# Optimization experiments

Measured on AMD Instinct MI355X. Metric: run time of the kernel, lower is better.

## Reference

```python
import jax, jax.numpy as jnp
import numpy as np

B, S, D = 4, 2048, 512
H, DK, DV = 8, 64, 64
ALPHA = 0.6
MAX_ITERS = 3
EPS = 1e-9


def setup_inputs() -> dict:
    key = jax.random.key(0)
    ks = jax.random.split(key, 9)
    scale = 1.0 / np.sqrt(D)
    return {
        "x": jax.random.normal(ks[0], (B, S, D), dtype=jnp.float32),
        "Wq": jax.random.normal(ks[1], (D, H * DK), dtype=jnp.float32) * scale,
        "bq": jnp.zeros((H * DK,), dtype=jnp.float32),
        "Wk": jax.random.normal(ks[2], (D, H * DK), dtype=jnp.float32) * scale,
        "bk": jnp.zeros((H * DK,), dtype=jnp.float32),
        "Wv": jax.random.normal(ks[3], (D, H * DV), dtype=jnp.float32) * scale,
        "bv": jnp.zeros((H * DV,), dtype=jnp.float32),
        "Wo": jax.random.normal(ks[4], (H * DV, D), dtype=jnp.float32) * scale,
        "bo": jnp.zeros((D,), dtype=jnp.float32),
    }


def reference(x, Wq, bq, Wk, bk, Wv, bv, Wo, bo):
    # QKV projections -> [B, H, S, dk]
    q = (x @ Wq + bq).reshape(B, S, H, DK).transpose(0, 2, 1, 3)
    k = (x @ Wk + bk).reshape(B, S, H, DK).transpose(0, 2, 1, 3)
    v = (x @ Wv + bv).reshape(B, S, H, DV).transpose(0, 2, 1, 3)

    # scaled dot-product scores: [B, H, S, S]
    scores = jnp.einsum("bhqd,bhkd->bhqk", q, k) / jnp.sqrt(jnp.float32(DK))
    w = jax.nn.softmax(scores, axis=-1)

    # iterative sparsification: threshold_t = 1 / (alpha^t * N), then renormalize
    n = jnp.float32(S)
    for t in range(MAX_ITERS):
        thr = 1.0 / ((ALPHA ** t) * n)
        w = jnp.where(w >= thr, w, 0.0)
        w = w / (jnp.sum(w, axis=-1, keepdims=True) + EPS)

    # attend and project out
    out = jnp.einsum("bhqk,bhkd->bhqd", w, v)          # [B, H, S, dv]
    out = out.transpose(0, 2, 1, 3).reshape(B, S, H * DV)
    return out @ Wo + bo
```

## Files before the change

kernel.cpp:

```cpp
#include <hip/hip_runtime.h>
#include <hip/hip_bf16.h>
#include <math.h>

#define NB 4
#define NS 2048
#define ND 512
#define NH 8
#define NDK 64
#define NDV 64

typedef __attribute__((ext_vector_type(8))) short short8;
typedef __attribute__((ext_vector_type(4))) float f32x4;

__device__ __forceinline__ unsigned short f2bfu(float f) {
  unsigned int u = __builtin_bit_cast(unsigned int, f);
  unsigned int rounding = 0x7fffu + ((u >> 16) & 1u);
  return (unsigned short)((u + rounding) >> 16);
}
__device__ __forceinline__ float bfu2f(unsigned short u) {
  return __builtin_bit_cast(float, (unsigned int)u << 16);
}


__global__ void k_make_xcat(const float* __restrict__ in, unsigned short* __restrict__ out,
                            int n4) {
  int i = blockIdx.x * 256 + threadIdx.x;
  if (i >= n4) return;
  int row = i >> 7, col = (i & 127) * 4;
  float4 f = reinterpret_cast<const float4*>(in)[i];
  ushort4 h, l;
  h.x = f2bfu(f.x); h.y = f2bfu(f.y); h.z = f2bfu(f.z); h.w = f2bfu(f.w);
  l.x = f2bfu(f.x - bfu2f(h.x)); l.y = f2bfu(f.y - bfu2f(h.y));
  l.z = f2bfu(f.z - bfu2f(h.z)); l.w = f2bfu(f.w - bfu2f(h.w));
  ushort4* o = reinterpret_cast<ushort4*>(out + (size_t)row * 1536);
  o[col / 4] = h;
  o[(col + 512) / 4] = h;
  o[(col + 1024) / 4] = l;
}

__global__ void k_transpose_split(const float* __restrict__ src, unsigned short* __restrict__ dst,
                                  int R, int C) {
  __shared__ float t[32][33];
  int bx = blockIdx.x * 32, by = blockIdx.y * 32;
  int tx = threadIdx.x, ty = threadIdx.y;
  for (int i = 0; i < 32; i += 8)
    t[ty + i][tx] = src[(size_t)(by + ty + i) * C + bx + tx];
  __syncthreads();
  for (int i = 0; i < 32; i += 8) {
    float f = t[tx][ty + i];
    unsigned short h = f2bfu(f);
    unsigned short l = f2bfu(f - bfu2f(h));
    size_t base = (size_t)(bx + ty + i) * (3 * R) + by + tx;
    dst[base] = h;
    dst[base + R] = l;
    dst[base + 2 * R] = h;
  }
}

template <int MODE>
__global__ __launch_bounds__(256) void k_gemm_nt(
    const unsigned short* __restrict__ A, const unsigned short* __restrict__ Bt,
    const float* __restrict__ bias, void* __restrict__ outp, unsigned short* __restrict__ outlo,
    int M, int N, int K) {
  __shared__ __align__(16) unsigned short As[64][88];
  __shared__ __align__(16) unsigned short Bs[64][88];
  const int tid = threadIdx.x;
  const int m0 = blockIdx.y * 64;
  const int n0 = blockIdx.x * 64;
  const int wave = tid >> 6, lane = tid & 63;
  const int lm = lane & 15, lg = lane >> 4;

  f32x4 acc[4];
  for (int n = 0; n < 4; n++) acc[n] = (f32x4){0.f, 0.f, 0.f, 0.f};

  for (int k0 = 0; k0 < K; k0 += 64) {
    for (int it = 0; it < 2; it++) {
      int c = tid + it * 256;
      int row = c >> 3, col = (c & 7) * 8;
      *reinterpret_cast<short8*>(&As[row][col]) =
          *reinterpret_cast<const short8*>(A + (size_t)(m0 + row) * K + k0 + col);
      *reinterpret_cast<short8*>(&Bs[row][col]) =
          *reinterpret_cast<const short8*>(Bt + (size_t)(n0 + row) * K + k0 + col);
    }
    __syncthreads();
#pragma unroll
    for (int ks = 0; ks < 2; ks++) {
      short8 a = *reinterpret_cast<const short8*>(&As[wave * 16 + lm][ks * 32 + lg * 8]);
#pragma unroll
      for (int n = 0; n < 4; n++) {
        short8 b = *reinterpret_cast<const short8*>(&Bs[n * 16 + lm][ks * 32 + lg * 8]);
        acc[n] = __builtin_amdgcn_mfma_f32_16x16x32_bf16(a, b, acc[n], 0, 0, 0);
      }
    }
    __syncthreads();
  }

#pragma unroll
  for (int n = 0; n < 4; n++) {
    int gn = n0 + n * 16 + lm;
    float bv = bias[gn];
#pragma unroll
    for (int r = 0; r < 4; r++) {
      int gm = m0 + wave * 16 + lg * 4 + r;
      float v = acc[n][r] + bv;
      if (MODE == 3) {
        reinterpret_cast<float*>(outp)[(size_t)gm * ND + gn] = v;
      } else {
        int b = gm >> 11, s = gm & (NS - 1);
        int h = gn >> 6, d = gn & 63;
        unsigned short hb = f2bfu(v);
        unsigned short lb = f2bfu(v - bfu2f(hb));
        size_t idx;
        if (MODE == 0)
          idx = (((size_t)b * NH + h) * NS + s) * NDK + d;
        else
          idx = (((size_t)b * NH + h) * NDV + d) * NS + s;
        reinterpret_cast<unsigned short*>(outp)[idx] = hb;
        outlo[idx] = lb;
      }
    }
  }
}

__global__ __launch_bounds__(1024) void k_sparse_attn(
    const unsigned short* __restrict__ Qh, const unsigned short* __restrict__ Ql,
    const unsigned short* __restrict__ Kh, const unsigned short* __restrict__ Kl,
    const unsigned short* __restrict__ Vth, const unsigned short* __restrict__ Vtl,
    unsigned short* __restrict__ attn) {
  __shared__ __align__(16) float sc[16][2052];
  __shared__ __align__(16) float red[4][4][16][16];
  __shared__ float rowcut[16], rowinv[16];

  const int tid = threadIdx.x;
  const int wave = tid >> 6, lane = tid & 63;
  const int lm = lane & 15, lg = lane >> 4;

  const int orig = blockIdx.x;
  const int blk = (orig & 7) * 512 + (orig >> 3);
  const int qt = blk & (NS / 16 - 1);
  const int bh = blk >> 7;
  const int q0 = qt * 16;

  const size_t qoff = ((size_t)bh * NS + q0) * NDK;
  const unsigned short* Kph = Kh + (size_t)bh * NS * NDK;
  const unsigned short* Kpl = Kl + (size_t)bh * NS * NDK;
  const unsigned short* Vph = Vth + (size_t)bh * NDV * NS;
  const unsigned short* Vpl = Vtl + (size_t)bh * NDV * NS;

  {
    short8 qh0 = *reinterpret_cast<const short8*>(Qh + qoff + lm * NDK + lg * 8);
    short8 qh1 = *reinterpret_cast<const short8*>(Qh + qoff + lm * NDK + 32 + lg * 8);
    short8 ql0 = *reinterpret_cast<const short8*>(Ql + qoff + lm * NDK + lg * 8);
    short8 ql1 = *reinterpret_cast<const short8*>(Ql + qoff + lm * NDK + 32 + lg * 8);
#pragma unroll
    for (int it = 0; it < 8; it++) {
      int t0 = wave * 128 + it * 16;
      f32x4 a = (f32x4){0.f, 0.f, 0.f, 0.f};
      size_t ko = (size_t)t0 * NDK;
      short8 bh0 = *reinterpret_cast<const short8*>(Kph + ko + lm * NDK + lg * 8);
      short8 bh1 = *reinterpret_cast<const short8*>(Kph + ko + lm * NDK + 32 + lg * 8);
      short8 bl0 = *reinterpret_cast<const short8*>(Kpl + ko + lm * NDK + lg * 8);
      short8 bl1 = *reinterpret_cast<const short8*>(Kpl + ko + lm * NDK + 32 + lg * 8);
      a = __builtin_amdgcn_mfma_f32_16x16x32_bf16(qh0, bh0, a, 0, 0, 0);
      a = __builtin_amdgcn_mfma_f32_16x16x32_bf16(qh1, bh1, a, 0, 0, 0);
      a = __builtin_amdgcn_mfma_f32_16x16x32_bf16(qh0, bl0, a, 0, 0, 0);
      a = __builtin_amdgcn_mfma_f32_16x16x32_bf16(qh1, bl1, a, 0, 0, 0);
      a = __builtin_amdgcn_mfma_f32_16x16x32_bf16(ql0, bh0, a, 0, 0, 0);
      a = __builtin_amdgcn_mfma_f32_16x16x32_bf16(ql1, bh1, a, 0, 0, 0);
#pragma unroll
      for (int r = 0; r < 4; r++)
        sc[lg * 4 + r][t0 + lm] = a[r] * 0.125f;
    }
  }
  __syncthreads();

  {
    const float thr[3] = {1.0f / 2048.0f, 1.0f / (0.6f * 2048.0f), 1.0f / (0.36f * 2048.0f)};
    const int row = wave;
    float m = -1e30f;
    for (int i = lane; i < NS; i += 64) m = fmaxf(m, sc[row][i]);
    for (int s = 32; s > 0; s >>= 1) m = fmaxf(m, __shfl_xor(m, s));
    float E = 0.f;
    for (int i = lane; i < NS; i += 64) {
      float e = __expf(sc[row][i] - m);
      sc[row][i] = e;
      E += e;
    }
    for (int s = 32; s > 0; s >>= 1) E += __shfl_xor(E, s);
    float Dd = 1.0f, cutE = 0.f;
#pragma unroll
    for (int t = 0; t < 3; t++) {
      cutE = fmaxf(cutE, thr[t] * Dd * E);
      float Ssum = 0.f;
      for (int i = lane; i < NS; i += 64) {
        float e = sc[row][i];
        if (e >= cutE) Ssum += e;
      }
      for (int s = 32; s > 0; s >>= 1) Ssum += __shfl_xor(Ssum, s);
      Dd = Ssum / E + 1e-9f * Dd;
    }
    if (lane == 0) {
      rowcut[row] = cutE;
      rowinv[row] = 1.0f / (E * Dd);
    }
  }
  __syncthreads();

  {
    const int d = wave & 3;
    const int kk = wave >> 2;
    const float cut = rowcut[lm], inv = rowinv[lm];
    const unsigned short* vph = Vph + (size_t)(d * 16 + lm) * NS + kk * 512;
    const unsigned short* vpl = Vpl + (size_t)(d * 16 + lm) * NS + kk * 512;
    f32x4 pacc = (f32x4){0.f, 0.f, 0.f, 0.f};
#pragma unroll
    for (int ks = 0; ks < 16; ks++) {
      int c = kk * 512 + ks * 32 + lg * 8;
      f32x4 e0 = *reinterpret_cast<const f32x4*>(&sc[lm][c]);
      f32x4 e1 = *reinterpret_cast<const f32x4*>(&sc[lm][c + 4]);
      short8 ah, al;
#pragma unroll
      for (int j = 0; j < 4; j++) {
        float w0 = (e0[j] >= cut) ? e0[j] * inv : 0.f;
        unsigned short h0 = f2bfu(w0);
        ah[j] = (short)h0; al[j] = (short)f2bfu(w0 - bfu2f(h0));
        float w1 = (e1[j] >= cut) ? e1[j] * inv : 0.f;
        unsigned short h1 = f2bfu(w1);
        ah[4 + j] = (short)h1; al[4 + j] = (short)f2bfu(w1 - bfu2f(h1));
      }
      short8 vh = *reinterpret_cast<const short8*>(vph + ks * 32 + lg * 8);
      short8 vl = *reinterpret_cast<const short8*>(vpl + ks * 32 + lg * 8);
      pacc = __builtin_amdgcn_mfma_f32_16x16x32_bf16(ah, vh, pacc, 0, 0, 0);
      pacc = __builtin_amdgcn_mfma_f32_16x16x32_bf16(ah, vl, pacc, 0, 0, 0);
      pacc = __builtin_amdgcn_mfma_f32_16x16x32_bf16(al, vh, pacc, 0, 0, 0);
    }
#pragma unroll
    for (int r = 0; r < 4; r++) red[kk][d][lg * 4 + r][lm] = pacc[r];
  }
  __syncthreads();

  if (wave < 4) {
    const int d = wave;
    const int b = bh >> 3, h = bh & 7;
#pragma unroll
    for (int r = 0; r < 4; r++) {
      int q = lg * 4 + r;
      float v = red[0][d][q][lm] + red[1][d][q][lm] + red[2][d][q][lm] + red[3][d][q][lm];
      int s = q0 + q;
      int c = h * 64 + d * 16 + lm;
      unsigned short hb = f2bfu(v);
      unsigned short lb = f2bfu(v - bfu2f(hb));
      size_t base = ((size_t)b * NS + s) * 1536;
      attn[base + c] = hb;
      attn[base + c + 512] = hb;
      attn[base + c + 1024] = lb;
    }
  }
}


extern "C" void kernel_launch(void* const* d_in, const int* in_sizes, int n_in,
                              void* d_out, int out_size, void* d_ws, size_t ws_size,
                              hipStream_t stream) {
  const float* x  = (const float*)d_in[0];
  const float* Wq = (const float*)d_in[1];
  const float* bq = (const float*)d_in[2];
  const float* Wk = (const float*)d_in[3];
  const float* bk = (const float*)d_in[4];
  const float* Wv = (const float*)d_in[5];
  const float* bv = (const float*)d_in[6];
  const float* Wo = (const float*)d_in[7];
  const float* bo = (const float*)d_in[8];

  char* ws = (char*)d_ws;
  size_t off = 0;
  auto alloc = [&](size_t bytes) {
    char* p = ws + off;
    off += (bytes + 255) & ~(size_t)255;
    return p;
  };
  const int M = NB * NS;
  unsigned short* xcat = (unsigned short*)alloc((size_t)M * 1536 * 2);
  unsigned short* wqC  = (unsigned short*)alloc((size_t)512 * 1536 * 2);
  unsigned short* wkC  = (unsigned short*)alloc((size_t)512 * 1536 * 2);
  unsigned short* wvC  = (unsigned short*)alloc((size_t)512 * 1536 * 2);
  unsigned short* woC  = (unsigned short*)alloc((size_t)512 * 1536 * 2);
  unsigned short* Qhi  = (unsigned short*)alloc((size_t)M * 512 * 2);
  unsigned short* Qlo  = (unsigned short*)alloc((size_t)M * 512 * 2);
  unsigned short* Khi  = (unsigned short*)alloc((size_t)M * 512 * 2);
  unsigned short* Klo  = (unsigned short*)alloc((size_t)M * 512 * 2);
  unsigned short* Vthi = (unsigned short*)alloc((size_t)M * 512 * 2);
  unsigned short* Vtlo = (unsigned short*)alloc((size_t)M * 512 * 2);
  unsigned short* attn = xcat;

  k_make_xcat<<<(M * 512 / 4 + 255) / 256, 256, 0, stream>>>(x, xcat, M * 512 / 4);

  dim3 tg(16, 16), tb(32, 8);
  k_transpose_split<<<tg, tb, 0, stream>>>(Wq, wqC, ND, NH * NDK);
  k_transpose_split<<<tg, tb, 0, stream>>>(Wk, wkC, ND, NH * NDK);
  k_transpose_split<<<tg, tb, 0, stream>>>(Wv, wvC, ND, NH * NDV);
  k_transpose_split<<<tg, tb, 0, stream>>>(Wo, woC, NH * NDV, ND);

  dim3 gg(512 / 64, M / 64);
  k_gemm_nt<0><<<gg, 256, 0, stream>>>(xcat, wqC, bq, Qhi, Qlo, M, 512, 1536);
  k_gemm_nt<0><<<gg, 256, 0, stream>>>(xcat, wkC, bk, Khi, Klo, M, 512, 1536);
  k_gemm_nt<2><<<gg, 256, 0, stream>>>(xcat, wvC, bv, Vthi, Vtlo, M, 512, 1536);

  k_sparse_attn<<<NB * NH * (NS / 16), 1024, 0, stream>>>(Qhi, Qlo, Khi, Klo, Vthi, Vtlo, attn);

  k_gemm_nt<3><<<gg, 256, 0, stream>>>(attn, woC, bo, d_out, nullptr, M, 512, 1536);
}
```

Baseline: 976.1 us.

## Keep softmax rows in registers and precompute split-bf16 probabilities in LDS

Each wave now loads its score row into registers once and does the max, exp, and three threshold passes without rereading shared memory. The normalized, split-bf16 probabilities are written back into the score buffer, so the PV stage reads them directly instead of recomputing the threshold and conversion in every wave. The QK stage swaps the MFMA operands to get vectorized f32x4 stores, and both matmul stages use independent accumulators to break MFMA dependency chains. The cost is higher register pressure from holding 32 floats per lane at 1024 threads per block.

```diff
diff --git a/kernel.cpp b/kernel.cpp
--- a/kernel.cpp
+++ b/kernel.cpp
@@ -129,7 +129,6 @@
     unsigned short* __restrict__ attn) {
   __shared__ __align__(16) float sc[16][2052];
   __shared__ __align__(16) float red[4][4][16][16];
-  __shared__ float rowcut[16], rowinv[16];
 
   const int tid = threadIdx.x;
   const int wave = tid >> 6, lane = tid & 63;
@@ -153,55 +152,97 @@
     short8 ql0 = *reinterpret_cast<const short8*>(Ql + qoff + lm * NDK + lg * 8);
     short8 ql1 = *reinterpret_cast<const short8*>(Ql + qoff + lm * NDK + 32 + lg * 8);
 #pragma unroll
-    for (int it = 0; it < 8; it++) {
-      int t0 = wave * 128 + it * 16;
-      f32x4 a = (f32x4){0.f, 0.f, 0.f, 0.f};
-      size_t ko = (size_t)t0 * NDK;
-      short8 bh0 = *reinterpret_cast<const short8*>(Kph + ko + lm * NDK + lg * 8);
-      short8 bh1 = *reinterpret_cast<const short8*>(Kph + ko + lm * NDK + 32 + lg * 8);
-      short8 bl0 = *reinterpret_cast<const short8*>(Kpl + ko + lm * NDK + lg * 8);
-      short8 bl1 = *reinterpret_cast<const short8*>(Kpl + ko + lm * NDK + 32 + lg * 8);
-      a = __builtin_amdgcn_mfma_f32_16x16x32_bf16(qh0, bh0, a, 0, 0, 0);
-      a = __builtin_amdgcn_mfma_f32_16x16x32_bf16(qh1, bh1, a, 0, 0, 0);
-      a = __builtin_amdgcn_mfma_f32_16x16x32_bf16(qh0, bl0, a, 0, 0, 0);
-      a = __builtin_amdgcn_mfma_f32_16x16x32_bf16(qh1, bl1, a, 0, 0, 0);
-      a = __builtin_amdgcn_mfma_f32_16x16x32_bf16(ql0, bh0, a, 0, 0, 0);
-      a = __builtin_amdgcn_mfma_f32_16x16x32_bf16(ql1, bh1, a, 0, 0, 0);
-#pragma unroll
-      for (int r = 0; r < 4; r++)
-        sc[lg * 4 + r][t0 + lm] = a[r] * 0.125f;
+    for (int it = 0; it < 8; it += 2) {
+      int t0a = wave * 128 + it * 16;
+      int t0b = t0a + 16;
+      size_t koa = (size_t)t0a * NDK, kob = (size_t)t0b * NDK;
+      short8 ah0 = *reinterpret_cast<const short8*>(Kph + koa + lm * NDK + lg * 8);
+      short8 ah1 = *reinterpret_cast<const short8*>(Kph + koa + lm * NDK + 32 + lg * 8);
+      short8 al0 = *reinterpret_cast<const short8*>(Kpl + koa + lm * NDK + lg * 8);
+      short8 al1 = *reinterpret_cast<const short8*>(Kpl + koa + lm * NDK + 32 + lg * 8);
+      short8 bh0 = *reinterpret_cast<const short8*>(Kph + kob + lm * NDK + lg * 8);
+      short8 bh1 = *reinterpret_cast<const short8*>(Kph + kob + lm * NDK + 32 + lg * 8);
+      short8 bl0 = *reinterpret_cast<const short8*>(Kpl + kob + lm * NDK + lg * 8);
+      short8 bl1 = *reinterpret_cast<const short8*>(Kpl + kob + lm * NDK + 32 + lg * 8);
+      {
+        f32x4 a0 = (f32x4){0.f, 0.f, 0.f, 0.f};
+        f32x4 a1 = (f32x4){0.f, 0.f, 0.f, 0.f};
+        a0 = __builtin_amdgcn_mfma_f32_16x16x32_bf16(ah0, qh0, a0, 0, 0, 0);
+        a1 = __builtin_amdgcn_mfma_f32_16x16x32_bf16(ah1, qh1, a1, 0, 0, 0);
+        a0 = __builtin_amdgcn_mfma_f32_16x16x32_bf16(al0, qh0, a0, 0, 0, 0);
+        a1 = __builtin_amdgcn_mfma_f32_16x16x32_bf16(al1, qh1, a1, 0, 0, 0);
+        a0 = __builtin_amdgcn_mfma_f32_16x16x32_bf16(ah0, ql0, a0, 0, 0, 0);
+        a1 = __builtin_amdgcn_mfma_f32_16x16x32_bf16(ah1, ql1, a1, 0, 0, 0);
+        f32x4 v = (a0 + a1) * 0.125f;
+        *reinterpret_cast<f32x4*>(&sc[lm][t0a + lg * 4]) = v;
+      }
+      {
+        f32x4 a0 = (f32x4){0.f, 0.f, 0.f, 0.f};
+        f32x4 a1 = (f32x4){0.f, 0.f, 0.f, 0.f};
+        a0 = __builtin_amdgcn_mfma_f32_16x16x32_bf16(bh0, qh0, a0, 0, 0, 0);
+        a1 = __builtin_amdgcn_mfma_f32_16x16x32_bf16(bh1, qh1, a1, 0, 0, 0);
+        a0 = __builtin_amdgcn_mfma_f32_16x16x32_bf16(bl0, qh0, a0, 0, 0, 0);
+        a1 = __builtin_amdgcn_mfma_f32_16x16x32_bf16(bl1, qh1, a1, 0, 0, 0);
+        a0 = __builtin_amdgcn_mfma_f32_16x16x32_bf16(bh0, ql0, a0, 0, 0, 0);
+        a1 = __builtin_amdgcn_mfma_f32_16x16x32_bf16(bh1, ql1, a1, 0, 0, 0);
+        f32x4 v = (a0 + a1) * 0.125f;
+        *reinterpret_cast<f32x4*>(&sc[lm][t0b + lg * 4]) = v;
+      }
     }
   }
   __syncthreads();
 
   {
     const float thr[3] = {1.0f / 2048.0f, 1.0f / (0.6f * 2048.0f), 1.0f / (0.36f * 2048.0f)};
-    const int row = wave;
+    char* rb = (char*)&sc[wave][0];
+    f32x4 ev[8];
+#pragma unroll
+    for (int it = 0; it < 8; it++)
+      ev[it] = *reinterpret_cast<const f32x4*>(rb + 4 * (it * 256 + lane * 4));
     float m = -1e30f;
-    for (int i = lane; i < NS; i += 64) m = fmaxf(m, sc[row][i]);
+#pragma unroll
+    for (int it = 0; it < 8; it++)
+      m = fmaxf(m, fmaxf(fmaxf(ev[it][0], ev[it][1]), fmaxf(ev[it][2], ev[it][3])));
     for (int s = 32; s > 0; s >>= 1) m = fmaxf(m, __shfl_xor(m, s));
     float E = 0.f;
-    for (int i = lane; i < NS; i += 64) {
-      float e = __expf(sc[row][i] - m);
-      sc[row][i] = e;
-      E += e;
+#pragma unroll
+    for (int it = 0; it < 8; it++) {
+#pragma unroll
+      for (int j = 0; j < 4; j++) {
+        float e = __expf(ev[it][j] - m);
+        ev[it][j] = e;
+        E += e;
+      }
     }
     for (int s = 32; s > 0; s >>= 1) E += __shfl_xor(E, s);
-    float Dd = 1.0f, cutE = 0.f;
+    float Dd = 1.0f, cut = 0.f;
 #pragma unroll
     for (int t = 0; t < 3; t++) {
-      cutE = fmaxf(cutE, thr[t] * Dd * E);
+      cut = fmaxf(cut, thr[t] * Dd * E);
       float Ssum = 0.f;
-      for (int i = lane; i < NS; i += 64) {
-        float e = sc[row][i];
-        if (e >= cutE) Ssum += e;
+#pragma unroll
+      for (int it = 0; it < 8; it++) {
+#pragma unroll
+        for (int j = 0; j < 4; j++) Ssum += (ev[it][j] >= cut) ? ev[it][j] : 0.f;
       }
       for (int s = 32; s > 0; s >>= 1) Ssum += __shfl_xor(Ssum, s);
       Dd = Ssum / E + 1e-9f * Dd;
     }
-    if (lane == 0) {
-      rowcut[row] = cutE;
-      rowinv[row] = 1.0f / (E * Dd);
+    const float inv = 1.0f / (E * Dd);
+#pragma unroll
+    for (int it = 0; it < 8; it++) {
+      ushort4 hv, lv;
+#pragma unroll
+      for (int j = 0; j < 4; j++) {
+        float e = ev[it][j];
+        float w = (e >= cut) ? e * inv : 0.f;
+        unsigned short h = f2bfu(w);
+        (&hv.x)[j] = h;
+        (&lv.x)[j] = f2bfu(w - bfu2f(h));
+      }
+      int c = it * 256 + lane * 4;
+      *reinterpret_cast<ushort4*>(rb + 2 * c) = hv;
+      *reinterpret_cast<ushort4*>(rb + 4096 + 2 * c) = lv;
     }
   }
   __syncthreads();
@@ -209,31 +250,31 @@
   {
     const int d = wave & 3;
     const int kk = wave >> 2;
-    const float cut = rowcut[lm], inv = rowinv[lm];
     const unsigned short* vph = Vph + (size_t)(d * 16 + lm) * NS + kk * 512;
     const unsigned short* vpl = Vpl + (size_t)(d * 16 + lm) * NS + kk * 512;
-    f32x4 pacc = (f32x4){0.f, 0.f, 0.f, 0.f};
-#pragma unroll
-    for (int ks = 0; ks < 16; ks++) {
-      int c = kk * 512 + ks * 32 + lg * 8;
-      f32x4 e0 = *reinterpret_cast<const f32x4*>(&sc[lm][c]);
-      f32x4 e1 = *reinterpret_cast<const f32x4*>(&sc[lm][c + 4]);
-      short8 ah, al;
-#pragma unroll
-      for (int j = 0; j < 4; j++) {
-        float w0 = (e0[j] >= cut) ? e0[j] * inv : 0.f;
-        unsigned short h0 = f2bfu(w0);
-        ah[j] = (short)h0; al[j] = (short)f2bfu(w0 - bfu2f(h0));
-        float w1 = (e1[j] >= cut) ? e1[j] * inv : 0.f;
-        unsigned short h1 = f2bfu(w1);
-        ah[4 + j] = (short)h1; al[4 + j] = (short)f2bfu(w1 - bfu2f(h1));
-      }
-      short8 vh = *reinterpret_cast<const short8*>(vph + ks * 32 + lg * 8);
-      short8 vl = *reinterpret_cast<const short8*>(vpl + ks * 32 + lg * 8);
-      pacc = __builtin_amdgcn_mfma_f32_16x16x32_bf16(ah, vh, pacc, 0, 0, 0);
-      pacc = __builtin_amdgcn_mfma_f32_16x16x32_bf16(ah, vl, pacc, 0, 0, 0);
-      pacc = __builtin_amdgcn_mfma_f32_16x16x32_bf16(al, vh, pacc, 0, 0, 0);
-    }
+    const char* prow = (const char*)&sc[lm][0];
+    f32x4 acc0 = (f32x4){0.f, 0.f, 0.f, 0.f};
+    f32x4 acc1 = (f32x4){0.f, 0.f, 0.f, 0.f};
+    f32x4 acc2 = (f32x4){0.f, 0.f, 0.f, 0.f};
+#pragma unroll
+    for (int ks = 0; ks < 16; ks += 2) {
+      int c0 = kk * 512 + ks * 32 + lg * 8;
+      short8 vh0 = *reinterpret_cast<const short8*>(vph + ks * 32 + lg * 8);
+      short8 vl0 = *reinterpret_cast<const short8*>(vpl + ks * 32 + lg * 8);
+      short8 vh1 = *reinterpret_cast<const short8*>(vph + (ks + 1) * 32 + lg * 8);
+      short8 vl1 = *reinterpret_cast<const short8*>(vpl + (ks + 1) * 32 + lg * 8);
+      short8 ph0 = *reinterpret_cast<const short8*>(prow + 2 * c0);
+      short8 pl0 = *reinterpret_cast<const short8*>(prow + 4096 + 2 * c0);
+      short8 ph1 = *reinterpret_cast<const short8*>(prow + 2 * (c0 + 32));
+      short8 pl1 = *reinterpret_cast<const short8*>(prow + 4096 + 2 * (c0 + 32));
+      acc0 = __builtin_amdgcn_mfma_f32_16x16x32_bf16(ph0, vh0, acc0, 0, 0, 0);
+      acc1 = __builtin_amdgcn_mfma_f32_16x16x32_bf16(ph0, vl0, acc1, 0, 0, 0);
+      acc2 = __builtin_amdgcn_mfma_f32_16x16x32_bf16(pl0, vh0, acc2, 0, 0, 0);
+      acc0 = __builtin_amdgcn_mfma_f32_16x16x32_bf16(ph1, vh1, acc0, 0, 0, 0);
+      acc1 = __builtin_amdgcn_mfma_f32_16x16x32_bf16(ph1, vl1, acc1, 0, 0, 0);
+      acc2 = __builtin_amdgcn_mfma_f32_16x16x32_bf16(pl1, vh1, acc2, 0, 0, 0);
+    }
+    f32x4 pacc = (acc0 + acc1) + acc2;
 #pragma unroll
     for (int r = 0; r < 4; r++) red[kk][d][lg * 4 + r][lm] = pacc[r];
   }
```

Result: faster. 899.6 us (-7.8%).

## Keep attention scores in registers and drop the 128KB shared score buffer

Applied to the files above, without the earlier changes.

The sparse attention kernel no longer stages the 16x2048 score tile in shared memory. Each of 8 waves keeps its 256-key slice of transposed scores in registers, and cross-wave max, sum and threshold reductions go through a small shared partial buffer. The P matrix is rearranged into MFMA operand layout with lane shuffles, and each wave computes all 64 output dims over its key slice before a shared reduction. Freeing shared memory lets several blocks share a CU, in exchange for higher register pressure, more barriers and many shuffles.

```diff
diff --git a/kernel.cpp b/kernel.cpp
--- a/kernel.cpp
+++ b/kernel.cpp
@@ -11,6 +11,7 @@
 
 typedef __attribute__((ext_vector_type(8))) short short8;
 typedef __attribute__((ext_vector_type(4))) float f32x4;
+typedef __attribute__((ext_vector_type(4))) unsigned int u32x4;
 
 __device__ __forceinline__ unsigned short f2bfu(float f) {
   unsigned int u = __builtin_bit_cast(unsigned int, f);
@@ -122,14 +123,13 @@
   }
 }
 
-__global__ __launch_bounds__(1024) void k_sparse_attn(
+__global__ __launch_bounds__(512, 4) void k_sparse_attn(
     const unsigned short* __restrict__ Qh, const unsigned short* __restrict__ Ql,
     const unsigned short* __restrict__ Kh, const unsigned short* __restrict__ Kl,
     const unsigned short* __restrict__ Vth, const unsigned short* __restrict__ Vtl,
     unsigned short* __restrict__ attn) {
-  __shared__ __align__(16) float sc[16][2052];
-  __shared__ __align__(16) float red[4][4][16][16];
-  __shared__ float rowcut[16], rowinv[16];
+  __shared__ float part[5][8][16];
+  __shared__ __align__(16) float red[8][16][68];
 
   const int tid = threadIdx.x;
   const int wave = tid >> 6, lane = tid & 63;
@@ -146,111 +146,168 @@
   const unsigned short* Kpl = Kl + (size_t)bh * NS * NDK;
   const unsigned short* Vph = Vth + (size_t)bh * NDV * NS;
   const unsigned short* Vpl = Vtl + (size_t)bh * NDV * NS;
-
+  const int kvbase = wave * 256;
+
+  f32x4 st[16];
   {
     short8 qh0 = *reinterpret_cast<const short8*>(Qh + qoff + lm * NDK + lg * 8);
     short8 qh1 = *reinterpret_cast<const short8*>(Qh + qoff + lm * NDK + 32 + lg * 8);
     short8 ql0 = *reinterpret_cast<const short8*>(Ql + qoff + lm * NDK + lg * 8);
     short8 ql1 = *reinterpret_cast<const short8*>(Ql + qoff + lm * NDK + 32 + lg * 8);
 #pragma unroll
-    for (int it = 0; it < 8; it++) {
-      int t0 = wave * 128 + it * 16;
-      f32x4 a = (f32x4){0.f, 0.f, 0.f, 0.f};
-      size_t ko = (size_t)t0 * NDK;
-      short8 bh0 = *reinterpret_cast<const short8*>(Kph + ko + lm * NDK + lg * 8);
-      short8 bh1 = *reinterpret_cast<const short8*>(Kph + ko + lm * NDK + 32 + lg * 8);
-      short8 bl0 = *reinterpret_cast<const short8*>(Kpl + ko + lm * NDK + lg * 8);
-      short8 bl1 = *reinterpret_cast<const short8*>(Kpl + ko + lm * NDK + 32 + lg * 8);
-      a = __builtin_amdgcn_mfma_f32_16x16x32_bf16(qh0, bh0, a, 0, 0, 0);
-      a = __builtin_amdgcn_mfma_f32_16x16x32_bf16(qh1, bh1, a, 0, 0, 0);
-      a = __builtin_amdgcn_mfma_f32_16x16x32_bf16(qh0, bl0, a, 0, 0, 0);
-      a = __builtin_amdgcn_mfma_f32_16x16x32_bf16(qh1, bl1, a, 0, 0, 0);
-      a = __builtin_amdgcn_mfma_f32_16x16x32_bf16(ql0, bh0, a, 0, 0, 0);
-      a = __builtin_amdgcn_mfma_f32_16x16x32_bf16(ql1, bh1, a, 0, 0, 0);
-#pragma unroll
-      for (int r = 0; r < 4; r++)
-        sc[lg * 4 + r][t0 + lm] = a[r] * 0.125f;
-    }
+    for (int kt = 0; kt < 16; kt++) {
+      size_t ko = (size_t)(kvbase + kt * 16) * NDK;
+      const unsigned short* kh = Kph + ko + lm * NDK + lg * 8;
+      const unsigned short* kl = Kpl + ko + lm * NDK + lg * 8;
+      short8 ah0 = *reinterpret_cast<const short8*>(kh);
+      short8 ah1 = *reinterpret_cast<const short8*>(kh + 32);
+      short8 al0 = *reinterpret_cast<const short8*>(kl);
+      short8 al1 = *reinterpret_cast<const short8*>(kl + 32);
+      f32x4 a0 = (f32x4){0.f, 0.f, 0.f, 0.f};
+      f32x4 a1 = (f32x4){0.f, 0.f, 0.f, 0.f};
+      a0 = __builtin_amdgcn_mfma_f32_16x16x32_bf16(ah0, qh0, a0, 0, 0, 0);
+      a1 = __builtin_amdgcn_mfma_f32_16x16x32_bf16(ah1, qh1, a1, 0, 0, 0);
+      a0 = __builtin_amdgcn_mfma_f32_16x16x32_bf16(al0, qh0, a0, 0, 0, 0);
+      a1 = __builtin_amdgcn_mfma_f32_16x16x32_bf16(al1, qh1, a1, 0, 0, 0);
+      a0 = __builtin_amdgcn_mfma_f32_16x16x32_bf16(ah0, ql0, a0, 0, 0, 0);
+      a1 = __builtin_amdgcn_mfma_f32_16x16x32_bf16(ah1, ql1, a1, 0, 0, 0);
+      st[kt] = (a0 + a1) * 0.125f;
+    }
+  }
+
+  float cut, inv;
+  {
+    float m = -1e30f;
+#pragma unroll
+    for (int kt = 0; kt < 16; kt++)
+      m = fmaxf(m, fmaxf(fmaxf(st[kt][0], st[kt][1]), fmaxf(st[kt][2], st[kt][3])));
+    m = fmaxf(m, __shfl_xor(m, 16));
+    m = fmaxf(m, __shfl_xor(m, 32));
+    if (lg == 0) part[0][wave][lm] = m;
+    __syncthreads();
+    float gm = -1e30f;
+#pragma unroll
+    for (int w = 0; w < 8; w++) gm = fmaxf(gm, part[0][w][lm]);
+
+    float E = 0.f;
+#pragma unroll
+    for (int kt = 0; kt < 16; kt++) {
+#pragma unroll
+      for (int j = 0; j < 4; j++) {
+        float e = __expf(st[kt][j] - gm);
+        st[kt][j] = e;
+        E += e;
+      }
+    }
+    E += __shfl_xor(E, 16);
+    E += __shfl_xor(E, 32);
+    if (lg == 0) part[1][wave][lm] = E;
+    __syncthreads();
+    float gE = 0.f;
+#pragma unroll
+    for (int w = 0; w < 8; w++) gE += part[1][w][lm];
+
+    const float thr[3] = {1.0f / 2048.0f, 1.0f / (0.6f * 2048.0f), 1.0f / (0.36f * 2048.0f)};
+    float Dd = 1.0f;
+    cut = 0.f;
+#pragma unroll
+    for (int t = 0; t < 3; t++) {
+      cut = fmaxf(cut, thr[t] * Dd * gE);
+      float S = 0.f;
+#pragma unroll
+      for (int kt = 0; kt < 16; kt++) {
+#pragma unroll
+        for (int j = 0; j < 4; j++) S += (st[kt][j] >= cut) ? st[kt][j] : 0.f;
+      }
+      S += __shfl_xor(S, 16);
+      S += __shfl_xor(S, 32);
+      if (lg == 0) part[2 + t][wave][lm] = S;
+      __syncthreads();
+      float gS = 0.f;
+#pragma unroll
+      for (int w = 0; w < 8; w++) gS += part[2 + t][w][lm];
+      Dd = gS / gE + 1e-9f * Dd;
+    }
+    inv = 1.0f / (gE * Dd);
+  }
+
+  unsigned int Hp[16][2], Lp[16][2];
+#pragma unroll
+  for (int kt = 0; kt < 16; kt++) {
+#pragma unroll
+    for (int rp = 0; rp < 2; rp++) {
+      float w0 = st[kt][2 * rp], w1 = st[kt][2 * rp + 1];
+      w0 = (w0 >= cut) ? w0 * inv : 0.f;
+      w1 = (w1 >= cut) ? w1 * inv : 0.f;
+      unsigned int h0 = f2bfu(w0), h1 = f2bfu(w1);
+      Hp[kt][rp] = h0 | (h1 << 16);
+      unsigned int l0 = f2bfu(w0 - bfu2f((unsigned short)h0));
+      unsigned int l1 = f2bfu(w1 - bfu2f((unsigned short)h1));
+      Lp[kt][rp] = l0 | (l1 << 16);
+    }
+  }
+
+  {
+    const int e_lane = lm + 32 * (lg & 1);
+    const int o_lane = e_lane + 16;
+    const bool selB = (lane & 32) != 0;
+    f32x4 acc[4];
+#pragma unroll
+    for (int dt = 0; dt < 4; dt++) acc[dt] = (f32x4){0.f, 0.f, 0.f, 0.f};
+#pragma unroll
+    for (int wi = 0; wi < 8; wi++) {
+      unsigned int a0 = (unsigned)__shfl((int)Hp[2 * wi][0], e_lane);
+      unsigned int a1 = (unsigned)__shfl((int)Hp[2 * wi][1], e_lane);
+      unsigned int a2 = (unsigned)__shfl((int)Hp[2 * wi][0], o_lane);
+      unsigned int a3 = (unsigned)__shfl((int)Hp[2 * wi][1], o_lane);
+      unsigned int b0 = (unsigned)__shfl((int)Hp[2 * wi + 1][0], e_lane);
+      unsigned int b1 = (unsigned)__shfl((int)Hp[2 * wi + 1][1], e_lane);
+      unsigned int b2 = (unsigned)__shfl((int)Hp[2 * wi + 1][0], o_lane);
+      unsigned int b3 = (unsigned)__shfl((int)Hp[2 * wi + 1][1], o_lane);
+      u32x4 hw = (u32x4){selB ? b0 : a0, selB ? b1 : a1, selB ? b2 : a2, selB ? b3 : a3};
+      a0 = (unsigned)__shfl((int)Lp[2 * wi][0], e_lane);
+      a1 = (unsigned)__shfl((int)Lp[2 * wi][1], e_lane);
+      a2 = (unsigned)__shfl((int)Lp[2 * wi][0], o_lane);
+      a3 = (unsigned)__shfl((int)Lp[2 * wi][1], o_lane);
+      b0 = (unsigned)__shfl((int)Lp[2 * wi + 1][0], e_lane);
+      b1 = (unsigned)__shfl((int)Lp[2 * wi + 1][1], e_lane);
+      b2 = (unsigned)__shfl((int)Lp[2 * wi + 1][0], o_lane);
+      b3 = (unsigned)__shfl((int)Lp[2 * wi + 1][1], o_lane);
+      u32x4 lw = (u32x4){selB ? b0 : a0, selB ? b1 : a1, selB ? b2 : a2, selB ? b3 : a3};
+      short8 Ah = __builtin_bit_cast(short8, hw);
+      short8 Al = __builtin_bit_cast(short8, lw);
+      const int co = kvbase + wi * 32 + lg * 8;
+#pragma unroll
+      for (int dt = 0; dt < 4; dt++) {
+        short8 V0 = *reinterpret_cast<const short8*>(Vph + (size_t)(dt * 16 + lm) * NS + co);
+        short8 V1 = *reinterpret_cast<const short8*>(Vpl + (size_t)(dt * 16 + lm) * NS + co);
+        acc[dt] = __builtin_amdgcn_mfma_f32_16x16x32_bf16(Ah, V0, acc[dt], 0, 0, 0);
+        acc[dt] = __builtin_amdgcn_mfma_f32_16x16x32_bf16(Ah, V1, acc[dt], 0, 0, 0);
+        acc[dt] = __builtin_amdgcn_mfma_f32_16x16x32_bf16(Al, V0, acc[dt], 0, 0, 0);
+      }
+    }
+#pragma unroll
+    for (int dt = 0; dt < 4; dt++)
+#pragma unroll
+      for (int rr = 0; rr < 4; rr++) red[wave][lg * 4 + rr][dt * 16 + lm] = acc[dt][rr];
   }
   __syncthreads();
 
   {
-    const float thr[3] = {1.0f / 2048.0f, 1.0f / (0.6f * 2048.0f), 1.0f / (0.36f * 2048.0f)};
-    const int row = wave;
-    float m = -1e30f;
-    for (int i = lane; i < NS; i += 64) m = fmaxf(m, sc[row][i]);
-    for (int s = 32; s > 0; s >>= 1) m = fmaxf(m, __shfl_xor(m, s));
-    float E = 0.f;
-    for (int i = lane; i < NS; i += 64) {
-      float e = __expf(sc[row][i] - m);
-      sc[row][i] = e;
-      E += e;
-    }
-    for (int s = 32; s > 0; s >>= 1) E += __shfl_xor(E, s);
-    float Dd = 1.0f, cutE = 0.f;
-#pragma unroll
-    for (int t = 0; t < 3; t++) {
-      cutE = fmaxf(cutE, thr[t] * Dd * E);
-      float Ssum = 0.f;
-      for (int i = lane; i < NS; i += 64) {
-        float e = sc[row][i];
-        if (e >= cutE) Ssum += e;
-      }
-      for (int s = 32; s > 0; s >>= 1) Ssum += __shfl_xor(Ssum, s);
-      Dd = Ssum / E + 1e-9f * Dd;
-    }
-    if (lane == 0) {
-      rowcut[row] = cutE;
-      rowinv[row] = 1.0f / (E * Dd);
-    }
-  }
-  __syncthreads();
-
-  {
-    const int d = wave & 3;
-    const int kk = wave >> 2;
-    const float cut = rowcut[lm], inv = rowinv[lm];
-    const unsigned short* vph = Vph + (size_t)(d * 16 + lm) * NS + kk * 512;
-    const unsigned short* vpl = Vpl + (size_t)(d * 16 + lm) * NS + kk * 512;
-    f32x4 pacc = (f32x4){0.f, 0.f, 0.f, 0.f};
-#pragma unroll
-    for (int ks = 0; ks < 16; ks++) {
-      int c = kk * 512 + ks * 32 + lg * 8;
-      f32x4 e0 = *reinterpret_cast<const f32x4*>(&sc[lm][c]);
-      f32x4 e1 = *reinterpret_cast<const f32x4*>(&sc[lm][c + 4]);
-      short8 ah, al;
-#pragma unroll
-      for (int j = 0; j < 4; j++) {
-        float w0 = (e0[j] >= cut) ? e0[j] * inv : 0.f;
-        unsigned short h0 = f2bfu(w0);
-        ah[j] = (short)h0; al[j] = (short)f2bfu(w0 - bfu2f(h0));
-        float w1 = (e1[j] >= cut) ? e1[j] * inv : 0.f;
-        unsigned short h1 = f2bfu(w1);
-        ah[4 + j] = (short)h1; al[4 + j] = (short)f2bfu(w1 - bfu2f(h1));
-      }
-      short8 vh = *reinterpret_cast<const short8*>(vph + ks * 32 + lg * 8);
-      short8 vl = *reinterpret_cast<const short8*>(vpl + ks * 32 + lg * 8);
-      pacc = __builtin_amdgcn_mfma_f32_16x16x32_bf16(ah, vh, pacc, 0, 0, 0);
-      pacc = __builtin_amdgcn_mfma_f32_16x16x32_bf16(ah, vl, pacc, 0, 0, 0);
-      pacc = __builtin_amdgcn_mfma_f32_16x16x32_bf16(al, vh, pacc, 0, 0, 0);
-    }
-#pragma unroll
-    for (int r = 0; r < 4; r++) red[kk][d][lg * 4 + r][lm] = pacc[r];
-  }
-  __syncthreads();
-
-  if (wave < 4) {
-    const int d = wave;
+    const int q = tid >> 5;
+    const int dv0 = (tid & 31) * 2;
     const int b = bh >> 3, h = bh & 7;
-#pragma unroll
-    for (int r = 0; r < 4; r++) {
-      int q = lg * 4 + r;
-      float v = red[0][d][q][lm] + red[1][d][q][lm] + red[2][d][q][lm] + red[3][d][q][lm];
-      int s = q0 + q;
-      int c = h * 64 + d * 16 + lm;
+    const int s = q0 + q;
+    size_t base = ((size_t)b * NS + s) * 1536;
+#pragma unroll
+    for (int k2 = 0; k2 < 2; k2++) {
+      int dv = dv0 + k2;
+      float v = 0.f;
+#pragma unroll
+      for (int w = 0; w < 8; w++) v += red[w][q][dv];
+      int c = h * 64 + dv;
       unsigned short hb = f2bfu(v);
       unsigned short lb = f2bfu(v - bfu2f(hb));
-      size_t base = ((size_t)b * NS + s) * 1536;
       attn[base + c] = hb;
       attn[base + c + 512] = hb;
       attn[base + c + 1024] = lb;
@@ -306,7 +363,7 @@
   k_gemm_nt<0><<<gg, 256, 0, stream>>>(xcat, wkC, bk, Khi, Klo, M, 512, 1536);
   k_gemm_nt<2><<<gg, 256, 0, stream>>>(xcat, wvC, bv, Vthi, Vtlo, M, 512, 1536);
 
-  k_sparse_attn<<<NB * NH * (NS / 16), 1024, 0, stream>>>(Qhi, Qlo, Khi, Klo, Vthi, Vtlo, attn);
+  k_sparse_attn<<<NB * NH * (NS / 16), 512, 0, stream>>>(Qhi, Qlo, Khi, Klo, Vthi, Vtlo, attn);
 
   k_gemm_nt<3><<<gg, 256, 0, stream>>>(attn, woC, bo, d_out, nullptr, M, 512, 1536);
 }
```

After: 805.5 us. 17.5% less time.
